# Optimization experiments

Hardware: AMD Instinct MI355X
Metric: run time of the kernel (lower is better)

Reference implementation:

```python
import jax, jax.numpy as jnp
import numpy as np

B, S, D = 8, 4096, 1024


def setup_inputs() -> dict:
    key = jax.random.key(0)
    k = jax.random.split(key, 6)
    scale = 1.0 / np.sqrt(D)  # torch nn.Linear default init range
    x = jax.random.normal(k[0], (B, S, D), dtype=jnp.float32)
    mask = jnp.ones((B, S), dtype=jnp.float32)
    Wu = jax.random.uniform(k[1], (D, D), jnp.float32, -scale, scale)
    bu = jax.random.uniform(k[2], (D,), jnp.float32, -scale, scale)
    Wf = jax.random.uniform(k[3], (D, D), jnp.float32, -scale, scale)
    bf = jax.random.uniform(k[4], (D,), jnp.float32, -scale, scale)
    decay_param = jnp.zeros((1,), dtype=jnp.float32)
    return {"x": x, "mask": mask, "Wu": Wu, "bu": bu, "Wf": Wf, "bf": bf, "decay_param": decay_param}


def reference(x, mask, Wu, bu, Wf, bf, decay_param):
    # decay is a learned scalar in (0,1)
    decay = jax.nn.sigmoid(decay_param)[0]
    # Batch linear_update over all timesteps at once: (B,S,D)
    upd = jnp.einsum('bsd,ed->bse', x, Wu) + bu
    m = mask[..., None]  # (B,S,1)
    # mask-gated recurrence: mem_t = a_t * mem_{t-1} + b_t
    #   a_t = mask*decay + (1-mask),  b_t = mask*update
    a = m * decay + (1.0 - m)
    b = m * upd
    a_s = jnp.swapaxes(a, 0, 1)  # (S,B,1)
    b_s = jnp.swapaxes(b, 0, 1)  # (S,B,D)

    def step(mem, ab):
        a_t, b_t = ab
        mem = a_t * mem + b_t
        return mem, mem

    mem0 = jnp.zeros((B, D), dtype=x.dtype)
    _, mem_seq = jax.lax.scan(step, mem0, (a_s, b_s))  # (S,B,D)
    mem_seq = jnp.swapaxes(mem_seq, 0, 1)  # (B,S,D)
    # Batch linear_f over all timesteps
    out = jnp.einsum('bsd,ed->bse', mem_seq, Wf) + bf
    return out
```

## Files before the change

### kernel.cpp

```cpp
#include <hip/hip_runtime.h>
#include <hip/hip_bf16.h>
#include <math.h>

#define PB 8
#define PS 4096
#define PD 1024

typedef __attribute__((ext_vector_type(8))) short bf16x8;
typedef __attribute__((ext_vector_type(4))) float f32x4;

__device__ __forceinline__ ushort f2b(float f) {
    unsigned u = __float_as_uint(f);
    unsigned r = (u + 0x7FFFu + ((u >> 16) & 1u)) >> 16;
    return (ushort)r;
}
__device__ __forceinline__ float b2f(ushort h) {
    return __uint_as_float(((unsigned)h) << 16);
}

__device__ __forceinline__ void gl2lds16(const void* g, void* l) {
    __builtin_amdgcn_global_load_lds(
        (const __attribute__((address_space(1))) void*)g,
        (__attribute__((address_space(3))) void*)l, 16, 0, 0);
}

__global__ __launch_bounds__(256) void cvt_f32_bf16(const float* __restrict__ in,
                                                    ushort* __restrict__ out, int n) {
    int i = (blockIdx.x * 256 + threadIdx.x) * 4;
    if (i + 3 < n) {
        float4 v = *(const float4*)(in + i);
        ushort4 o;
        o.x = f2b(v.x); o.y = f2b(v.y); o.z = f2b(v.z); o.w = f2b(v.w);
        *(ushort4*)(out + i) = o;
    }
}

__global__ __launch_bounds__(256) void cvt_w2(const float* __restrict__ Wu,
                                              const float* __restrict__ Wf,
                                              ushort* __restrict__ Wub,
                                              ushort* __restrict__ Wfb, int n) {
    int i = (blockIdx.x * 256 + threadIdx.x) * 4;
    const float* in = (i < n) ? Wu : Wf;
    ushort* out = (i < n) ? Wub : Wfb;
    int j = (i < n) ? i : i - n;
    float4 v = *(const float4*)(in + j);
    ushort4 o;
    o.x = f2b(v.x); o.y = f2b(v.y); o.z = f2b(v.z); o.w = f2b(v.w);
    *(ushort4*)(out + j) = o;
}

template <bool OUT_BF16>
__global__ __launch_bounds__(256) void gemm_bt(const ushort* __restrict__ A,
                                               const ushort* __restrict__ Bm,
                                               const float* __restrict__ bias,
                                               void* __restrict__ C,
                                               int M, int N, int K) {
    __shared__ ushort As[128 * 32];
    __shared__ ushort Bs[128 * 32];

    const int tid = threadIdx.x;
    const int lane = tid & 63;
    const int wave = tid >> 6;
    const int nbn = N >> 7;
    const int xcd = blockIdx.x & 7;
    const int g = blockIdx.x >> 3;
    const int bm = xcd * ((M >> 7) >> 3) + g / nbn;
    const int bn = g % nbn;
    const int wm = wave >> 1, wn = wave & 1;
    const int l15 = lane & 15, quad = lane >> 4;

    const int grow = wave * 16 + (lane >> 2);
    const int gx = (lane & 3) ^ ((lane >> 3) & 3);
    const ushort* Ag = A + (size_t)(bm * 128 + grow) * K + gx * 8;
    const ushort* Bg = Bm + (size_t)(bn * 128 + grow) * K + gx * 8;
    ushort* Asw = As + wave * 512;
    ushort* Bsw = Bs + wave * 512;

    f32x4 acc[4][4];
#pragma unroll
    for (int i = 0; i < 4; ++i)
#pragma unroll
        for (int j = 0; j < 4; ++j) acc[i][j] = (f32x4){0.f, 0.f, 0.f, 0.f};

    const int rsw = (l15 >> 1) & 3;
    const int aoff = (quad ^ rsw) * 8;

    for (int k0 = 0; k0 < K; k0 += 32) {
        __syncthreads();
        gl2lds16(Ag + k0, Asw);
        gl2lds16(Ag + k0 + (size_t)64 * K, Asw + 2048);
        gl2lds16(Bg + k0, Bsw);
        gl2lds16(Bg + k0 + (size_t)64 * K, Bsw + 2048);
        __syncthreads();

        bf16x8 af[4], bfr[4];
#pragma unroll
        for (int i = 0; i < 4; ++i)
            af[i] = *(const bf16x8*)(As + (wm * 64 + i * 16 + l15) * 32 + aoff);
#pragma unroll
        for (int j = 0; j < 4; ++j)
            bfr[j] = *(const bf16x8*)(Bs + (wn * 64 + j * 16 + l15) * 32 + aoff);
#pragma unroll
        for (int i = 0; i < 4; ++i)
#pragma unroll
            for (int j = 0; j < 4; ++j)
                acc[i][j] = __builtin_amdgcn_mfma_f32_16x16x32_bf16(af[i], bfr[j], acc[i][j], 0, 0, 0);
    }

    const int gm0 = bm * 128 + wm * 64;
    const int gn0 = bn * 128 + wn * 64;
    float bv[4];
#pragma unroll
    for (int j = 0; j < 4; ++j) bv[j] = bias[gn0 + j * 16 + l15];
#pragma unroll
    for (int i = 0; i < 4; ++i) {
#pragma unroll
        for (int j = 0; j < 4; ++j) {
            const int col = gn0 + j * 16 + l15;
#pragma unroll
            for (int r = 0; r < 4; ++r) {
                const int row = gm0 + i * 16 + quad * 4 + r;
                float v = acc[i][j][r] + bv[j];
                if (OUT_BF16)
                    ((ushort*)C)[(size_t)row * N + col] = f2b(v);
                else
                    ((float*)C)[(size_t)row * N + col] = v;
            }
        }
    }
}

__global__ __launch_bounds__(256) void scan_partial(const ushort* __restrict__ upd,
                                                    const float* __restrict__ mask,
                                                    const float* __restrict__ dp,
                                                    float* __restrict__ Bc,
                                                    float* __restrict__ Ac,
                                                    int S, int D, int C) {
    const int c = blockIdx.x % C;
    const int b = blockIdx.x / C;
    const int L = S / C;
    const int d0 = threadIdx.x * 4;
    const float decay = 1.f / (1.f + expf(-dp[0]));
    const ushort* up = upd + ((size_t)b * S + (size_t)c * L) * D + d0;
    const float* mp = mask + (size_t)b * S + (size_t)c * L;
    float aA = 1.f;
    float b0 = 0.f, b1 = 0.f, b2 = 0.f, b3 = 0.f;
    for (int s = 0; s < L; ++s) {
        float m = mp[s];
        float a = m * decay + (1.f - m);
        ushort4 u = *(const ushort4*)(up + (size_t)s * D);
        aA *= a;
        b0 = a * b0 + m * b2f(u.x);
        b1 = a * b1 + m * b2f(u.y);
        b2 = a * b2 + m * b2f(u.z);
        b3 = a * b3 + m * b2f(u.w);
    }
    *(float4*)(Bc + (size_t)blockIdx.x * D + d0) = make_float4(b0, b1, b2, b3);
    if (threadIdx.x == 0) Ac[blockIdx.x] = aA;
}

__global__ __launch_bounds__(256) void scan_prefix(const float* __restrict__ Ac,
                                                   const float* __restrict__ Bc,
                                                   float* __restrict__ Mn, int D, int C) {
    int gid = blockIdx.x * 256 + threadIdx.x;
    int b = gid / D;
    int d = gid - b * D;
    float mem = 0.f;
    for (int c = 0; c < C; ++c) {
        size_t idx = ((size_t)(b * C + c)) * D + d;
        Mn[idx] = mem;
        mem = Ac[b * C + c] * mem + Bc[idx];
    }
}

__global__ __launch_bounds__(256) void scan_final(const ushort* __restrict__ upd,
                                                  const float* __restrict__ mask,
                                                  const float* __restrict__ dp,
                                                  const float* __restrict__ Mn,
                                                  ushort* __restrict__ ms,
                                                  int S, int D, int C) {
    const int c = blockIdx.x % C;
    const int b = blockIdx.x / C;
    const int L = S / C;
    const int d0 = threadIdx.x * 4;
    const float decay = 1.f / (1.f + expf(-dp[0]));
    const ushort* up = upd + ((size_t)b * S + (size_t)c * L) * D + d0;
    ushort* op = ms + ((size_t)b * S + (size_t)c * L) * D + d0;
    const float* mp = mask + (size_t)b * S + (size_t)c * L;
    float4 m0 = *(const float4*)(Mn + (size_t)blockIdx.x * D + d0);
    float v0 = m0.x, v1 = m0.y, v2 = m0.z, v3 = m0.w;
    for (int s = 0; s < L; ++s) {
        float m = mp[s];
        float a = m * decay + (1.f - m);
        ushort4 u = *(const ushort4*)(up + (size_t)s * D);
        v0 = a * v0 + m * b2f(u.x);
        v1 = a * v1 + m * b2f(u.y);
        v2 = a * v2 + m * b2f(u.z);
        v3 = a * v3 + m * b2f(u.w);
        ushort4 o;
        o.x = f2b(v0); o.y = f2b(v1); o.z = f2b(v2); o.w = f2b(v3);
        *(ushort4*)(op + (size_t)s * D) = o;
    }
}

extern "C" void kernel_launch(void* const* d_in, const int* in_sizes, int n_in,
                              void* d_out, int out_size, void* d_ws, size_t ws_size,
                              hipStream_t stream) {
    const float* x    = (const float*)d_in[0];
    const float* mask = (const float*)d_in[1];
    const float* Wu   = (const float*)d_in[2];
    const float* bu   = (const float*)d_in[3];
    const float* Wf   = (const float*)d_in[4];
    const float* bfv  = (const float*)d_in[5];
    const float* dp   = (const float*)d_in[6];

    const int B = PB, S = PS, D = PD;
    const int M = B * S;
    const int C = 64;

    char* ws = (char*)d_ws;
    ushort* xb   = (ushort*)(ws);
    ushort* updb = (ushort*)(ws + 67108864);
    ushort* memb = (ushort*)(ws + 134217728);
    ushort* Wub  = (ushort*)(ws + 201326592);
    ushort* Wfb  = (ushort*)(ws + 203423744);
    float*  Bc   = (float*)(ws + 205520896);
    float*  Mn   = (float*)(ws + 209715200);
    float*  Ac   = (float*)(ws + 213909504);

    const int nx = B * S * D;
    cvt_f32_bf16<<<nx / 1024, 256, 0, stream>>>(x, xb, nx);
    cvt_w2<<<(2 * D * D) / 1024, 256, 0, stream>>>(Wu, Wf, Wub, Wfb, D * D);

    dim3 g1((M / 128) * (D / 128));
    gemm_bt<true><<<g1, 256, 0, stream>>>(xb, Wub, bu, (void*)updb, M, D, D);

    scan_partial<<<B * C, 256, 0, stream>>>(updb, mask, dp, Bc, Ac, S, D, C);
    scan_prefix<<<(B * D) / 256, 256, 0, stream>>>(Ac, Bc, Mn, D, C);
    scan_final<<<B * C, 256, 0, stream>>>(updb, mask, dp, Mn, memb, S, D, C);

    gemm_bt<false><<<g1, 256, 0, stream>>>(memb, Wfb, bfv, d_out, M, D, D);
}
```

Before: 482.0 us.

## Double GEMM K-tile to 64 with XOR swizzle, unroll scan loops, more chunks

The GEMM now stages 64-wide K slices per iteration with an 8-way XOR swizzle, which halves the number of barrier-separated load/compute phases. The scan kernels unroll by four, batching update loads and vectorising the mask and carry loads to expose more memory parallelism. The chunk count rises from 64 to 128, giving more blocks for the partial and final scan passes at the cost of a longer serial prefix. LDS use per GEMM block doubles, which may reduce occupancy.

```diff
diff --git a/kernel.cpp b/kernel.cpp
--- a/kernel.cpp
+++ b/kernel.cpp
@@ -55,8 +55,8 @@
                                                const float* __restrict__ bias,
                                                void* __restrict__ C,
                                                int M, int N, int K) {
-    __shared__ ushort As[128 * 32];
-    __shared__ ushort Bs[128 * 32];
+    __shared__ ushort As[128 * 64];
+    __shared__ ushort Bs[128 * 64];
 
     const int tid = threadIdx.x;
     const int lane = tid & 63;
@@ -69,12 +69,12 @@
     const int wm = wave >> 1, wn = wave & 1;
     const int l15 = lane & 15, quad = lane >> 4;
 
-    const int grow = wave * 16 + (lane >> 2);
-    const int gx = (lane & 3) ^ ((lane >> 3) & 3);
-    const ushort* Ag = A + (size_t)(bm * 128 + grow) * K + gx * 8;
-    const ushort* Bg = Bm + (size_t)(bn * 128 + grow) * K + gx * 8;
-    ushort* Asw = As + wave * 512;
-    ushort* Bsw = Bs + wave * 512;
+    const int srow = wave * 8 + (lane >> 3);
+    const int sgx = ((lane & 7) ^ ((lane >> 3) & 7)) * 8;
+    const ushort* Ag = A + (size_t)(bm * 128 + srow) * K + sgx;
+    const ushort* Bg = Bm + (size_t)(bn * 128 + srow) * K + sgx;
+    ushort* Asw = As + wave * 8 * 64;
+    ushort* Bsw = Bs + wave * 8 * 64;
 
     f32x4 acc[4][4];
 #pragma unroll
@@ -82,29 +82,33 @@
 #pragma unroll
         for (int j = 0; j < 4; ++j) acc[i][j] = (f32x4){0.f, 0.f, 0.f, 0.f};
 
-    const int rsw = (l15 >> 1) & 3;
-    const int aoff = (quad ^ rsw) * 8;
-
-    for (int k0 = 0; k0 < K; k0 += 32) {
+    const int rsw = l15 & 7;
+
+    for (int k0 = 0; k0 < K; k0 += 64) {
         __syncthreads();
-        gl2lds16(Ag + k0, Asw);
-        gl2lds16(Ag + k0 + (size_t)64 * K, Asw + 2048);
-        gl2lds16(Bg + k0, Bsw);
-        gl2lds16(Bg + k0 + (size_t)64 * K, Bsw + 2048);
+#pragma unroll
+        for (int b = 0; b < 4; ++b) {
+            gl2lds16(Ag + k0 + (size_t)(b * 32) * K, Asw + b * 32 * 64);
+            gl2lds16(Bg + k0 + (size_t)(b * 32) * K, Bsw + b * 32 * 64);
+        }
         __syncthreads();
 
-        bf16x8 af[4], bfr[4];
-#pragma unroll
-        for (int i = 0; i < 4; ++i)
-            af[i] = *(const bf16x8*)(As + (wm * 64 + i * 16 + l15) * 32 + aoff);
-#pragma unroll
-        for (int j = 0; j < 4; ++j)
-            bfr[j] = *(const bf16x8*)(Bs + (wn * 64 + j * 16 + l15) * 32 + aoff);
-#pragma unroll
-        for (int i = 0; i < 4; ++i)
+#pragma unroll
+        for (int p = 0; p < 2; ++p) {
+            const int aoff = ((p * 4 + quad) ^ rsw) * 8;
+            bf16x8 af[4], bfr[4];
+#pragma unroll
+            for (int i = 0; i < 4; ++i)
+                af[i] = *(const bf16x8*)(As + (wm * 64 + i * 16 + l15) * 64 + aoff);
 #pragma unroll
             for (int j = 0; j < 4; ++j)
-                acc[i][j] = __builtin_amdgcn_mfma_f32_16x16x32_bf16(af[i], bfr[j], acc[i][j], 0, 0, 0);
+                bfr[j] = *(const bf16x8*)(Bs + (wn * 64 + j * 16 + l15) * 64 + aoff);
+#pragma unroll
+            for (int i = 0; i < 4; ++i)
+#pragma unroll
+                for (int j = 0; j < 4; ++j)
+                    acc[i][j] = __builtin_amdgcn_mfma_f32_16x16x32_bf16(af[i], bfr[j], acc[i][j], 0, 0, 0);
+        }
     }
 
     const int gm0 = bm * 128 + wm * 64;
@@ -145,15 +149,25 @@
     const float* mp = mask + (size_t)b * S + (size_t)c * L;
     float aA = 1.f;
     float b0 = 0.f, b1 = 0.f, b2 = 0.f, b3 = 0.f;
-    for (int s = 0; s < L; ++s) {
-        float m = mp[s];
-        float a = m * decay + (1.f - m);
-        ushort4 u = *(const ushort4*)(up + (size_t)s * D);
-        aA *= a;
-        b0 = a * b0 + m * b2f(u.x);
-        b1 = a * b1 + m * b2f(u.y);
-        b2 = a * b2 + m * b2f(u.z);
-        b3 = a * b3 + m * b2f(u.w);
+    for (int s0 = 0; s0 < L; s0 += 4) {
+        float4 mv = *(const float4*)(mp + s0);
+        ushort4 u0 = *(const ushort4*)(up + (size_t)(s0 + 0) * D);
+        ushort4 u1 = *(const ushort4*)(up + (size_t)(s0 + 1) * D);
+        ushort4 u2 = *(const ushort4*)(up + (size_t)(s0 + 2) * D);
+        ushort4 u3 = *(const ushort4*)(up + (size_t)(s0 + 3) * D);
+        float m, a;
+        m = mv.x; a = m * decay + (1.f - m); aA *= a;
+        b0 = a * b0 + m * b2f(u0.x); b1 = a * b1 + m * b2f(u0.y);
+        b2 = a * b2 + m * b2f(u0.z); b3 = a * b3 + m * b2f(u0.w);
+        m = mv.y; a = m * decay + (1.f - m); aA *= a;
+        b0 = a * b0 + m * b2f(u1.x); b1 = a * b1 + m * b2f(u1.y);
+        b2 = a * b2 + m * b2f(u1.z); b3 = a * b3 + m * b2f(u1.w);
+        m = mv.z; a = m * decay + (1.f - m); aA *= a;
+        b0 = a * b0 + m * b2f(u2.x); b1 = a * b1 + m * b2f(u2.y);
+        b2 = a * b2 + m * b2f(u2.z); b3 = a * b3 + m * b2f(u2.w);
+        m = mv.w; a = m * decay + (1.f - m); aA *= a;
+        b0 = a * b0 + m * b2f(u3.x); b1 = a * b1 + m * b2f(u3.y);
+        b2 = a * b2 + m * b2f(u3.z); b3 = a * b3 + m * b2f(u3.w);
     }
     *(float4*)(Bc + (size_t)blockIdx.x * D + d0) = make_float4(b0, b1, b2, b3);
     if (threadIdx.x == 0) Ac[blockIdx.x] = aA;
@@ -166,10 +180,17 @@
     int b = gid / D;
     int d = gid - b * D;
     float mem = 0.f;
-    for (int c = 0; c < C; ++c) {
-        size_t idx = ((size_t)(b * C + c)) * D + d;
-        Mn[idx] = mem;
-        mem = Ac[b * C + c] * mem + Bc[idx];
+    for (int c = 0; c < C; c += 4) {
+        float4 av = *(const float4*)(Ac + b * C + c);
+        size_t i0 = ((size_t)(b * C + c)) * D + d;
+        float q0 = Bc[i0];
+        float q1 = Bc[i0 + D];
+        float q2 = Bc[i0 + 2 * (size_t)D];
+        float q3 = Bc[i0 + 3 * (size_t)D];
+        Mn[i0] = mem;                    mem = av.x * mem + q0;
+        Mn[i0 + D] = mem;                mem = av.y * mem + q1;
+        Mn[i0 + 2 * (size_t)D] = mem;    mem = av.z * mem + q2;
+        Mn[i0 + 3 * (size_t)D] = mem;    mem = av.w * mem + q3;
     }
 }
 
@@ -189,17 +210,34 @@
     const float* mp = mask + (size_t)b * S + (size_t)c * L;
     float4 m0 = *(const float4*)(Mn + (size_t)blockIdx.x * D + d0);
     float v0 = m0.x, v1 = m0.y, v2 = m0.z, v3 = m0.w;
-    for (int s = 0; s < L; ++s) {
-        float m = mp[s];
-        float a = m * decay + (1.f - m);
-        ushort4 u = *(const ushort4*)(up + (size_t)s * D);
-        v0 = a * v0 + m * b2f(u.x);
-        v1 = a * v1 + m * b2f(u.y);
-        v2 = a * v2 + m * b2f(u.z);
-        v3 = a * v3 + m * b2f(u.w);
+    for (int s0 = 0; s0 < L; s0 += 4) {
+        float4 mv = *(const float4*)(mp + s0);
+        ushort4 u0 = *(const ushort4*)(up + (size_t)(s0 + 0) * D);
+        ushort4 u1 = *(const ushort4*)(up + (size_t)(s0 + 1) * D);
+        ushort4 u2 = *(const ushort4*)(up + (size_t)(s0 + 2) * D);
+        ushort4 u3 = *(const ushort4*)(up + (size_t)(s0 + 3) * D);
+        float m, a;
         ushort4 o;
-        o.x = f2b(v0); o.y = f2b(v1); o.z = f2b(v2); o.w = f2b(v3);
-        *(ushort4*)(op + (size_t)s * D) = o;
+        m = mv.x; a = m * decay + (1.f - m);
+        v0 = a * v0 + m * b2f(u0.x); v1 = a * v1 + m * b2f(u0.y);
+        v2 = a * v2 + m * b2f(u0.z); v3 = a * v3 + m * b2f(u0.w);
+        o.x = f2b(v0); o.y = f2b(v1); o.z = f2b(v2); o.w = f2b(v3);
+        *(ushort4*)(op + (size_t)(s0 + 0) * D) = o;
+        m = mv.y; a = m * decay + (1.f - m);
+        v0 = a * v0 + m * b2f(u1.x); v1 = a * v1 + m * b2f(u1.y);
+        v2 = a * v2 + m * b2f(u1.z); v3 = a * v3 + m * b2f(u1.w);
+        o.x = f2b(v0); o.y = f2b(v1); o.z = f2b(v2); o.w = f2b(v3);
+        *(ushort4*)(op + (size_t)(s0 + 1) * D) = o;
+        m = mv.z; a = m * decay + (1.f - m);
+        v0 = a * v0 + m * b2f(u2.x); v1 = a * v1 + m * b2f(u2.y);
+        v2 = a * v2 + m * b2f(u2.z); v3 = a * v3 + m * b2f(u2.w);
+        o.x = f2b(v0); o.y = f2b(v1); o.z = f2b(v2); o.w = f2b(v3);
+        *(ushort4*)(op + (size_t)(s0 + 2) * D) = o;
+        m = mv.w; a = m * decay + (1.f - m);
+        v0 = a * v0 + m * b2f(u3.x); v1 = a * v1 + m * b2f(u3.y);
+        v2 = a * v2 + m * b2f(u3.z); v3 = a * v3 + m * b2f(u3.w);
+        o.x = f2b(v0); o.y = f2b(v1); o.z = f2b(v2); o.w = f2b(v3);
+        *(ushort4*)(op + (size_t)(s0 + 3) * D) = o;
     }
 }
 
@@ -216,7 +254,7 @@
 
     const int B = PB, S = PS, D = PD;
     const int M = B * S;
-    const int C = 64;
+    const int C = 128;
 
     char* ws = (char*)d_ws;
     ushort* xb   = (ushort*)(ws);
```

Result: faster. 448.7 us (-6.9%).
